# Performance work log

Hardware: AMD Instinct MI355X
Metric: run time of the kernel (lower is better)

Reference implementation:

```python
import jax, jax.numpy as jnp
import numpy as np

N_ITEM, N_USER = 100000, 50000
D, H = 128, 8
DH = D // H
E1, E2 = 500000, 250000
NCNT = 51  # num_cnt_embeddings = cnt.max()+1
EPS = 1e-5


def setup_inputs() -> dict:
    key = jax.random.key(0)
    ks = jax.random.split(key, 32)
    r = lambda i, s: jax.random.normal(ks[i], s, dtype=jnp.float32)
    w = lambda i, s: jax.random.normal(ks[i], s, dtype=jnp.float32) * (1.0 / np.sqrt(s[-1]))
    return {
        # node features
        "ft_item": r(0, (N_ITEM, D)),
        "ft_user": r(1, (N_USER, D)),
        # hetero-level batch norm params (training-mode batch stats)
        "bn_g_item": jnp.ones((D,), jnp.float32), "bn_b_item": jnp.zeros((D,), jnp.float32),
        "bn_g_user": jnp.ones((D,), jnp.float32), "bn_b_user": jnp.zeros((D,), jnp.float32),
        # etype 'i2i' (item -> item), has cnt edge embedding
        "Wq1": w(2, (D, D)), "bq1": jnp.zeros((D,), jnp.float32),
        "Wk1": w(3, (D, D)), "Wv1": w(4, (D, D)),
        "ae1": r(5, (1, D)),
        "emb_cnt1": r(6, (NCNT, D)) * 0.1,
        # etype 'u2i' (user -> item), no cnt
        "Wq2": w(7, (D, D)), "bq2": jnp.zeros((D,), jnp.float32),
        "Wk2": w(8, (D, D)), "Wv2": w(9, (D, D)),
        "ae2": r(10, (1, D)),
        # vtype 'item' output transforms
        "W_agg": w(11, (D, D)), "b_agg": jnp.zeros((D,), jnp.float32),
        "W_self": w(12, (D, D)),
        # edges (eid order)
        "uid1": jax.random.randint(ks[13], (E1,), 0, N_ITEM, dtype=jnp.int32),
        "vid1": jax.random.randint(ks[14], (E1,), 0, N_ITEM, dtype=jnp.int32),
        "cnt1": jax.random.randint(ks[15], (E1,), 0, NCNT, dtype=jnp.int32),
        "uid2": jax.random.randint(ks[16], (E2,), 0, N_USER, dtype=jnp.int32),
        "vid2": jax.random.randint(ks[17], (E2,), 0, N_ITEM, dtype=jnp.int32),
    }


def _bn(x, g, b):
    mu = x.mean(0)
    var = x.var(0)
    return (x - mu) * jax.lax.rsqrt(var + EPS) * g + b


def _edge_scores(q_src, k_dst, uid, vid, attn_e, ft_e=None):
    # u_add_v gather, optional edge feature, gated per-head score [E, H]
    e = q_src[uid] + k_dst[vid]
    if ft_e is not None:
        e = e + ft_e
    e = attn_e * jax.nn.sigmoid(e)
    return e.reshape(-1, H, DH).sum(-1)


def reference(ft_item, ft_user, bn_g_item, bn_b_item, bn_g_user, bn_b_user,
              Wq1, bq1, Wk1, Wv1, ae1, emb_cnt1,
              Wq2, bq2, Wk2, Wv2, ae2,
              W_agg, b_agg, W_self,
              uid1, vid1, cnt1, uid2, vid2):
    xi = _bn(ft_item, bn_g_item, bn_b_item)   # item features (src and dst)
    xu = _bn(ft_user, bn_g_user, bn_b_user)   # user features (src only)

    # etype 'i2i': utype=item, vtype=item (ft_dst = xi, full graph)
    q1 = xi @ Wq1.T + bq1
    k1 = xi @ Wk1.T
    v1 = (xi @ Wv1.T).reshape(N_ITEM, H, DH)
    e1 = _edge_scores(q1, k1, uid1, vid1, ae1, ft_e=emb_cnt1[cnt1])  # [E1, H]

    # etype 'u2i': utype=user, vtype=item
    q2 = xu @ Wq2.T + bq2
    k2 = xi @ Wk2.T
    v2 = (xu @ Wv2.T).reshape(N_USER, H, DH)
    e2 = _edge_scores(q2, k2, uid2, vid2, ae2)  # [E2, H]

    # combined heterograph: offset user src ids by num item src nodes
    src = jnp.concatenate([uid1, uid2 + N_ITEM])
    dst = jnp.concatenate([vid1, vid2])
    val = jnp.concatenate([v1, v2], axis=0)        # [N_ITEM+N_USER, H, DH]
    sc = jnp.concatenate([e1, e2], axis=0)         # [E, H]

    # edge_softmax over incoming edges of each dst node (per head)
    m = jax.lax.stop_gradient(jax.ops.segment_max(sc, dst, num_segments=N_ITEM))
    ex = jnp.exp(sc - m[dst])
    s = jax.ops.segment_sum(ex, dst, num_segments=N_ITEM)
    a = ex / s[dst]                                # [E, H]

    # u_mul_e_sum: weighted scatter-sum of source values to dst
    agg = jax.ops.segment_sum(val[src] * a[:, :, None], dst,
                              num_segments=N_ITEM).reshape(N_ITEM, D)

    return jax.nn.relu(agg @ W_agg.T + b_agg + xi @ W_self.T)
```

## Files before the change

kernel.cpp:

```cpp
#include <hip/hip_runtime.h>
#include <hip/hip_bf16.h>

#define N_ITEM 100000
#define N_USER 50000
#define N_ALL  150000
#define E1N 500000
#define E2N 250000
#define EALL (E1N + E2N)
#define NPAD 100352

static constexpr size_t OFF_STATS = 0;
static constexpr size_t OFF_HIST  = 2048;
static constexpr size_t OFF_SCALE = OFF_HIST + (size_t)NPAD * 4;
static constexpr size_t OFF_M     = OFF_SCALE + 2048;
static constexpr size_t OFF_EMBB  = OFF_M + 64;
static constexpr size_t OFF_WPACK = OFF_EMBB + 13312;
static constexpr size_t OFF_QC    = OFF_WPACK + 8ull * 32768ull;
static constexpr size_t OFF_VC    = OFF_QC + (size_t)N_ALL * 256;
static constexpr size_t OFF_K1    = OFF_VC + (size_t)N_ALL * 256;
static constexpr size_t OFF_K2    = OFF_K1 + (size_t)N_ITEM * 256;
static constexpr size_t OFF_SELF  = OFF_K2 + (size_t)N_ITEM * 256;
static constexpr size_t OFF_START = OFF_SELF + (size_t)N_ITEM * 256;
static constexpr size_t OFF_CURSOR= OFF_START + (size_t)NPAD * 4;
static constexpr size_t OFF_BSUM  = OFF_CURSOR + (size_t)NPAD * 4;
static constexpr size_t OFF_ORD   = OFF_BSUM + 1024;
static constexpr size_t OFF_AGG   = OFF_ORD + (size_t)EALL * 8 + 128;

__device__ __forceinline__ float bf2f(unsigned short u) {
    return __uint_as_float(((unsigned)u) << 16);
}
__device__ __forceinline__ unsigned short f2bf(float f) {
    unsigned u = __float_as_uint(f);
    u += 0x7fffu + ((u >> 16) & 1u);
    return (unsigned short)(u >> 16);
}

typedef __attribute__((ext_vector_type(8))) short bf16x8;
typedef __attribute__((ext_vector_type(4))) float f32x4;

struct ProArgs {
    const float* w[8];
    const float* ft_item;
    const float* ft_user;
    const float* emb;
    const int* vid1;
    const int* vid2;
};
#define PRO_PACK 64
#define PRO_EMB  7
#define PRO_STAT 512
#define PRO_HIST 2930

__global__ __launch_bounds__(256) void prologue(ProArgs A, char* __restrict__ ws) {
    __shared__ float ls[256], ls2[256];
    int b = blockIdx.x, tid = threadIdx.x;
    if (b < PRO_PACK) {
        unsigned short* dst = (unsigned short*)(ws + OFF_WPACK);
        int gid = b * 256 + tid;
        int m = gid >> 11, rem = gid & 2047;
        int t = rem >> 8, kt = (rem >> 6) & 3, lane = rem & 63;
        int n = t * 16 + (lane & 15);
        int k0 = kt * 32 + (lane >> 4) * 8;
        const float* wrow = A.w[m] + n * 128 + k0;
        float4 w0 = *(const float4*)wrow;
        float4 w1 = *(const float4*)(wrow + 4);
        ushort4 o0 = make_ushort4(f2bf(w0.x), f2bf(w0.y), f2bf(w0.z), f2bf(w0.w));
        ushort4 o1 = make_ushort4(f2bf(w1.x), f2bf(w1.y), f2bf(w1.z), f2bf(w1.w));
        *(ushort4*)(dst + (size_t)gid * 8)     = o0;
        *(ushort4*)(dst + (size_t)gid * 8 + 4) = o1;
    } else if (b < PRO_PACK + PRO_EMB) {
        int gid = (b - PRO_PACK) * 256 + tid;
        if (gid * 4 < 51 * 128) {
            float4 v = *(const float4*)(A.emb + gid * 4);
            ushort4 o = make_ushort4(f2bf(v.x), f2bf(v.y), f2bf(v.z), f2bf(v.w));
            *(ushort4*)((unsigned short*)(ws + OFF_EMBB) + gid * 4) = o;
        }
    } else if (b < PRO_PACK + PRO_EMB + PRO_STAT) {
        int bb = b - PRO_PACK - PRO_EMB;
        int type = bb >> 8, xb = bb & 255;
        const float* x = type ? A.ft_user : A.ft_item;
        int N = type ? N_USER : N_ITEM;
        float* sum = (float*)(ws + OFF_STATS) + type * 256;
        float* sq  = sum + 128;
        int c = tid & 127;
        int half = tid >> 7;
        float s = 0.f, s2 = 0.f;
        for (int r = xb * 2 + half; r < N; r += 512) {
            float v = x[(size_t)r * 128 + c];
            s += v; s2 += v * v;
        }
        ls[tid] = s; ls2[tid] = s2;
        __syncthreads();
        if (half == 0) {
            atomicAdd(&sum[c], ls[c] + ls[c + 128]);
            atomicAdd(&sq[c],  ls2[c] + ls2[c + 128]);
        }
    } else {
        int e = (b - PRO_PACK - PRO_EMB - PRO_STAT) * 256 + tid;
        if (e < EALL) {
            int dst = (e < E1N) ? A.vid1[e] : A.vid2[e - E1N];
            atomicAdd((int*)(ws + OFF_HIST) + dst, 1);
        }
    }
}

__global__ __launch_bounds__(1024) void scan_partial(char* __restrict__ ws) {
    __shared__ int sd[1024];
    const int* hist = (const int*)(ws + OFF_HIST);
    int* start  = (int*)(ws + OFF_START);
    int* cursor = (int*)(ws + OFF_CURSOR);
    int* bsum   = (int*)(ws + OFF_BSUM);
    int t = threadIdx.x;
    int gid = blockIdx.x * 1024 + t;
    int v = hist[gid];
    sd[t] = v;
    __syncthreads();
    #pragma unroll
    for (int off = 1; off < 1024; off <<= 1) {
        int x = (t >= off) ? sd[t - off] : 0;
        __syncthreads();
        sd[t] += x;
        __syncthreads();
    }
    int ex = sd[t] - v;
    start[gid] = ex;
    cursor[gid] = ex;
    if (t == 1023) bsum[blockIdx.x] = sd[t];
}

__global__ __launch_bounds__(256) void mid(const float* __restrict__ g_i, const float* __restrict__ b_i,
                                           const float* __restrict__ g_u, const float* __restrict__ b_u,
                                           const float* __restrict__ ae1, const float* __restrict__ ae2,
                                           char* __restrict__ ws) {
    __shared__ int sd[128];
    int t = threadIdx.x;
    if (blockIdx.x == 0) {
        const float* stats = (const float*)(ws + OFF_STATS);
        float* scale = (float*)(ws + OFF_SCALE);
        float* M     = (float*)(ws + OFF_M);
        int type = t >> 7, c = t & 127;
        float N = type ? (float)N_USER : (float)N_ITEM;
        float su = stats[type * 256 + c];
        float sq = stats[type * 256 + 128 + c];
        float mu = su / N;
        float var = sq / N - mu * mu;
        float rstd = rsqrtf(var + 1e-5f);
        float g = type ? g_u[c] : g_i[c];
        float b = type ? b_u[c] : b_i[c];
        scale[type * 256 + c]       = g * rstd;
        scale[type * 256 + 128 + c] = b - mu * g * rstd;
        if (t < 8) {
            float m1 = 0.f, m2 = 0.f;
            for (int j = 0; j < 16; j++) {
                m1 += fmaxf(ae1[t * 16 + j], 0.f);
                m2 += fmaxf(ae2[t * 16 + j], 0.f);
            }
            M[t] = fmaxf(m1, m2);
        }
    } else {
        int* bsum = (int*)(ws + OFF_BSUM);
        int v = 0;
        if (t < 128) { v = (t < 98) ? bsum[t] : 0; sd[t] = v; }
        __syncthreads();
        #pragma unroll
        for (int off = 1; off < 128; off <<= 1) {
            int x = 0;
            if (t < 128 && t >= off) x = sd[t - off];
            __syncthreads();
            if (t < 128) sd[t] += x;
            __syncthreads();
        }
        if (t < 98) bsum[t] = sd[t] - v;
    }
}

__global__ __launch_bounds__(256) void edge_scatter(const int* __restrict__ uid1, const int* __restrict__ vid1,
                                                    const int* __restrict__ cnt1,
                                                    const int* __restrict__ uid2, const int* __restrict__ vid2,
                                                    char* __restrict__ ws) {
    int e = blockIdx.x * 256 + threadIdx.x;
    if (e >= EALL) return;
    int* cursor = (int*)(ws + OFF_CURSOR);
    const int* bsum = (const int*)(ws + OFF_BSUM);
    int2* ord = (int2*)(ws + OFF_ORD);
    int2 rec; int dst;
    if (e < E1N) {
        rec.x = uid1[e]; rec.y = cnt1[e]; dst = vid1[e];
    } else {
        int ee = e - E1N;
        rec.x = N_ITEM + uid2[ee]; rec.y = -1; dst = vid2[ee];
    }
    int pos = atomicAdd(&cursor[dst], 1) + bsum[dst >> 10];
    ord[pos] = rec;
}

struct TArgs {
    const float* x;
    const float* bias0;
    int N;
    int scaleOff;
    int nmat;
    int wtIdx[5];
    unsigned short* out[5];
};

#define TB_I 782
#define TB_U 391
#define SPITCH 136

__global__ __launch_bounds__(256, 5) void transform(TArgs AI, TArgs AU, char* __restrict__ ws) {
    __shared__ unsigned short stg[4][2][16 * SPITCH];
    int b = blockIdx.x;
    const TArgs& A = (b < TB_I) ? AI : AU;
    int blk = (b < TB_I) ? b : b - TB_I;

    const unsigned short* wpack = (const unsigned short*)(ws + OFF_WPACK);
    const float* scaleb = (const float*)(ws + OFF_SCALE) + A.scaleOff;
    int tid = threadIdx.x, lane = tid & 63, wv = tid >> 6;
    int l16 = lane & 15, quad = lane >> 4;
    int base = blk * 128 + wv * 32;

    bf16x8 bfr[2][4];
    #pragma unroll
    for (int kt = 0; kt < 4; kt++) {
        int c0 = kt * 32 + quad * 8;
        float4 sc0 = *(const float4*)(scaleb + c0);
        float4 sc1 = *(const float4*)(scaleb + c0 + 4);
        float4 bi0 = *(const float4*)(scaleb + 128 + c0);
        float4 bi1 = *(const float4*)(scaleb + 128 + c0 + 4);
        #pragma unroll
        for (int it = 0; it < 2; it++) {
            int gr = base + it * 16 + l16;
            bf16x8 f = {0, 0, 0, 0, 0, 0, 0, 0};
            if (gr < A.N) {
                const float* p = A.x + (size_t)gr * 128 + c0;
                float4 v0 = *(const float4*)p;
                float4 v1 = *(const float4*)(p + 4);
                f[0] = (short)f2bf(fmaf(v0.x, sc0.x, bi0.x));
                f[1] = (short)f2bf(fmaf(v0.y, sc0.y, bi0.y));
                f[2] = (short)f2bf(fmaf(v0.z, sc0.z, bi0.z));
                f[3] = (short)f2bf(fmaf(v0.w, sc0.w, bi0.w));
                f[4] = (short)f2bf(fmaf(v1.x, sc1.x, bi1.x));
                f[5] = (short)f2bf(fmaf(v1.y, sc1.y, bi1.y));
                f[6] = (short)f2bf(fmaf(v1.z, sc1.z, bi1.z));
                f[7] = (short)f2bf(fmaf(v1.w, sc1.w, bi1.w));
            }
            bfr[it][kt] = f;
        }
    }

    for (int m = 0; m < A.nmat; m++) {
        const unsigned short* wp = wpack + (size_t)A.wtIdx[m] * 16384;
        unsigned short* outp = A.out[m];
        const float* bias = (m == 0) ? A.bias0 : nullptr;
        #pragma unroll
        for (int it = 0; it < 2; it++) {
            unsigned short* st = stg[wv][it];
            #pragma unroll
            for (int nt = 0; nt < 8; nt++) {
                bf16x8 a4[4];
                #pragma unroll
                for (int kt = 0; kt < 4; kt++)
                    a4[kt] = *(const bf16x8*)(wp + (size_t)((nt * 4 + kt) * 64 + lane) * 8);
                f32x4 acc = {0.f, 0.f, 0.f, 0.f};
                if (bias) {
                    float4 bv = *(const float4*)(bias + nt * 16 + quad * 4);
                    acc[0] = bv.x; acc[1] = bv.y; acc[2] = bv.z; acc[3] = bv.w;
                }
                #pragma unroll
                for (int kt = 0; kt < 4; kt++)
                    acc = __builtin_amdgcn_mfma_f32_16x16x32_bf16(a4[kt], bfr[it][kt], acc, 0, 0, 0);
                ushort4 o = make_ushort4(f2bf(acc[0]), f2bf(acc[1]), f2bf(acc[2]), f2bf(acc[3]));
                *(ushort4*)(st + l16 * SPITCH + nt * 16 + quad * 4) = o;
            }
            #pragma unroll
            for (int i = 0; i < 4; i++) {
                int chunk = i * 64 + lane;
                int row = chunk >> 4, c8 = (chunk & 15) * 8;
                int gr = base + it * 16 + row;
                if (gr < A.N)
                    *(bf16x8*)(outp + (size_t)gr * 128 + c8) = *(const bf16x8*)(st + row * SPITCH + c8);
            }
        }
    }
}

__global__ __launch_bounds__(256, 8) void edge_agg(const float* __restrict__ ae1, const float* __restrict__ ae2,
                                                   char* __restrict__ ws) {
    const unsigned short* qc = (const unsigned short*)(ws + OFF_QC);
    const unsigned short* vc = (const unsigned short*)(ws + OFF_VC);
    const unsigned short* k1 = (const unsigned short*)(ws + OFF_K1);
    const unsigned short* k2 = (const unsigned short*)(ws + OFF_K2);
    const unsigned short* embb = (const unsigned short*)(ws + OFF_EMBB);
    const int* start = (const int*)(ws + OFF_START);
    const int* bsum  = (const int*)(ws + OFF_BSUM);
    const int2* ord = (const int2*)(ws + OFF_ORD);
    const float* M = (const float*)(ws + OFF_M);
    float* agg = (float*)(ws + OFF_AGG);

    int tid = threadIdx.x;
    int lane = tid & 63;
    int half = lane >> 5;
    int l = lane & 31;
    int d0 = l << 2;
    int h = l >> 2;
    int dst = blockIdx.x * 4 + (tid >> 6);
    if (dst >= N_ITEM) return;

    float mh = M[h];
    float4 ae1v = *(const float4*)(ae1 + d0);
    float4 ae2v = *(const float4*)(ae2 + d0);
    ushort4 k1p = *(const ushort4*)(k1 + (size_t)dst * 128 + d0);
    ushort4 k2p = *(const ushort4*)(k2 + (size_t)dst * 128 + d0);
    float4 k1v = make_float4(bf2f(k1p.x), bf2f(k1p.y), bf2f(k1p.z), bf2f(k1p.w));
    float4 k2v = make_float4(bf2f(k2p.x), bf2f(k2p.y), bf2f(k2p.z), bf2f(k2p.w));

    int beg = start[dst] + bsum[dst >> 10];
    int end = start[dst + 1] + bsum[(dst + 1) >> 10];
    float a0 = 0.f, a1 = 0.f, a2 = 0.f, a3 = 0.f, s = 0.f;

    int i = beg + half;
    if (i < end) {
        int2 rec = ord[i];
        while (true) {
            int inext = i + 2;
            int ipf = (inext < end) ? inext : (end - 1);
            int2 recn = ord[ipf];
            bool t1 = rec.y >= 0;
            ushort4 qp = *(const ushort4*)(qc + (size_t)rec.x * 128 + d0);
            ushort4 vp = *(const ushort4*)(vc + (size_t)rec.x * 128 + d0);
            ushort4 ep = *(const ushort4*)(embb + (size_t)(t1 ? rec.y : 0) * 128 + d0);
            float x0 = bf2f(qp.x) + (t1 ? k1v.x + bf2f(ep.x) : k2v.x);
            float x1 = bf2f(qp.y) + (t1 ? k1v.y + bf2f(ep.y) : k2v.y);
            float x2 = bf2f(qp.z) + (t1 ? k1v.z + bf2f(ep.z) : k2v.z);
            float x3 = bf2f(qp.w) + (t1 ? k1v.w + bf2f(ep.w) : k2v.w);
            float4 ae = t1 ? ae1v : ae2v;
            float t = ae.x * __builtin_amdgcn_rcpf(1.f + __expf(-x0))
                    + ae.y * __builtin_amdgcn_rcpf(1.f + __expf(-x1))
                    + ae.z * __builtin_amdgcn_rcpf(1.f + __expf(-x2))
                    + ae.w * __builtin_amdgcn_rcpf(1.f + __expf(-x3));
            t += __shfl_xor(t, 1);
            t += __shfl_xor(t, 2);
            float ex = __expf(t - mh);
            s += ex;
            a0 = fmaf(ex, bf2f(vp.x), a0);
            a1 = fmaf(ex, bf2f(vp.y), a1);
            a2 = fmaf(ex, bf2f(vp.z), a2);
            a3 = fmaf(ex, bf2f(vp.w), a3);
            if (inext >= end) break;
            i = inext; rec = recn;
        }
    }
    s  += __shfl_xor(s, 32);
    a0 += __shfl_xor(a0, 32);
    a1 += __shfl_xor(a1, 32);
    a2 += __shfl_xor(a2, 32);
    a3 += __shfl_xor(a3, 32);
    if (half == 0) {
        float inv = (s > 0.f) ? __builtin_amdgcn_rcpf(s) : 0.f;
        float4 o = make_float4(a0 * inv, a1 * inv, a2 * inv, a3 * inv);
        *(float4*)(agg + (size_t)dst * 128 + d0) = o;
    }
}

#define FPITCH 132

__global__ __launch_bounds__(256) void final_mfma(const float* __restrict__ b_agg,
                                                  float* __restrict__ out, char* __restrict__ ws) {
    __shared__ float stg[4][16 * FPITCH];
    const float* agg = (const float*)(ws + OFF_AGG);
    const unsigned short* selft = (const unsigned short*)(ws + OFF_SELF);
    const unsigned short* wp = (const unsigned short*)(ws + OFF_WPACK) + 7ull * 16384;
    int tid = threadIdx.x, lane = tid & 63, wv = tid >> 6;
    int l16 = lane & 15, quad = lane >> 4;
    int base = blockIdx.x * 256 + wv * 64;
    float* st = stg[wv];

    bf16x8 bfr[4][4];
    #pragma unroll
    for (int it = 0; it < 4; it++) {
        int gr = base + it * 16 + l16;
        #pragma unroll
        for (int kt = 0; kt < 4; kt++) {
            bf16x8 f = {0, 0, 0, 0, 0, 0, 0, 0};
            if (gr < N_ITEM) {
                const float* p = agg + (size_t)gr * 128 + kt * 32 + quad * 8;
                float4 v0 = *(const float4*)p;
                float4 v1 = *(const float4*)(p + 4);
                f[0] = (short)f2bf(v0.x); f[1] = (short)f2bf(v0.y);
                f[2] = (short)f2bf(v0.z); f[3] = (short)f2bf(v0.w);
                f[4] = (short)f2bf(v1.x); f[5] = (short)f2bf(v1.y);
                f[6] = (short)f2bf(v1.z); f[7] = (short)f2bf(v1.w);
            }
            bfr[it][kt] = f;
        }
    }

    #pragma unroll
    for (int it = 0; it < 4; it++) {
        #pragma unroll
        for (int nt = 0; nt < 8; nt++) {
            bf16x8 a4[4];
            #pragma unroll
            for (int kt = 0; kt < 4; kt++)
                a4[kt] = *(const bf16x8*)(wp + (size_t)((nt * 4 + kt) * 64 + lane) * 8);
            float4 bv = *(const float4*)(b_agg + nt * 16 + quad * 4);
            f32x4 acc = {bv.x, bv.y, bv.z, bv.w};
            #pragma unroll
            for (int kt = 0; kt < 4; kt++)
                acc = __builtin_amdgcn_mfma_f32_16x16x32_bf16(a4[kt], bfr[it][kt], acc, 0, 0, 0);
            *(f32x4*)(st + l16 * FPITCH + nt * 16 + quad * 4) = acc;
        }
        #pragma unroll
        for (int i = 0; i < 8; i++) {
            int chunk = i * 64 + lane;
            int row = chunk >> 5, c4 = (chunk & 31) * 4;
            int gr = base + it * 16 + row;
            if (gr < N_ITEM) {
                float4 v = *(const float4*)(st + row * FPITCH + c4);
                size_t idx = (size_t)gr * 128 + c4;
                ushort4 sf = *(const ushort4*)(selft + idx);
                float4 o;
                o.x = fmaxf(v.x + bf2f(sf.x), 0.f);
                o.y = fmaxf(v.y + bf2f(sf.y), 0.f);
                o.z = fmaxf(v.z + bf2f(sf.z), 0.f);
                o.w = fmaxf(v.w + bf2f(sf.w), 0.f);
                *(float4*)(out + idx) = o;
            }
        }
    }
}

extern "C" void kernel_launch(void* const* d_in, const int* in_sizes, int n_in,
                              void* d_out, int out_size, void* d_ws, size_t ws_size,
                              hipStream_t stream) {
    char* ws = (char*)d_ws;

    const float* ft_item = (const float*)d_in[0];
    const float* ft_user = (const float*)d_in[1];
    const float* bng_i = (const float*)d_in[2];
    const float* bnb_i = (const float*)d_in[3];
    const float* bng_u = (const float*)d_in[4];
    const float* bnb_u = (const float*)d_in[5];
    const float* Wq1 = (const float*)d_in[6];
    const float* bq1 = (const float*)d_in[7];
    const float* Wk1 = (const float*)d_in[8];
    const float* Wv1 = (const float*)d_in[9];
    const float* ae1 = (const float*)d_in[10];
    const float* emb = (const float*)d_in[11];
    const float* Wq2 = (const float*)d_in[12];
    const float* bq2 = (const float*)d_in[13];
    const float* Wk2 = (const float*)d_in[14];
    const float* Wv2 = (const float*)d_in[15];
    const float* ae2 = (const float*)d_in[16];
    const float* W_agg = (const float*)d_in[17];
    const float* b_agg = (const float*)d_in[18];
    const float* W_self = (const float*)d_in[19];
    const int* uid1 = (const int*)d_in[20];
    const int* vid1 = (const int*)d_in[21];
    const int* cnt1 = (const int*)d_in[22];
    const int* uid2 = (const int*)d_in[23];
    const int* vid2 = (const int*)d_in[24];
    float* out = (float*)d_out;

    hipMemsetAsync(ws + OFF_STATS, 0, 2048 + (size_t)NPAD * 4, stream);

    ProArgs pa;
    pa.w[0] = Wq1; pa.w[1] = Wk1; pa.w[2] = Wv1; pa.w[3] = Wk2;
    pa.w[4] = W_self; pa.w[5] = Wq2; pa.w[6] = Wv2; pa.w[7] = W_agg;
    pa.ft_item = ft_item; pa.ft_user = ft_user; pa.emb = emb;
    pa.vid1 = vid1; pa.vid2 = vid2;
    prologue<<<PRO_PACK + PRO_EMB + PRO_STAT + PRO_HIST, 256, 0, stream>>>(pa, ws);

    scan_partial<<<98, 1024, 0, stream>>>(ws);

    mid<<<2, 256, 0, stream>>>(bng_i, bnb_i, bng_u, bnb_u, ae1, ae2, ws);

    edge_scatter<<<(EALL + 255) / 256, 256, 0, stream>>>(uid1, vid1, cnt1, uid2, vid2, ws);

    TArgs ti, tu;
    ti.x = ft_item; ti.bias0 = bq1; ti.N = N_ITEM; ti.scaleOff = 0; ti.nmat = 5;
    ti.wtIdx[0] = 0; ti.wtIdx[1] = 1; ti.wtIdx[2] = 2; ti.wtIdx[3] = 3; ti.wtIdx[4] = 4;
    unsigned short* QC = (unsigned short*)(ws + OFF_QC);
    unsigned short* VC = (unsigned short*)(ws + OFF_VC);
    ti.out[0] = QC;
    ti.out[1] = (unsigned short*)(ws + OFF_K1);
    ti.out[2] = VC;
    ti.out[3] = (unsigned short*)(ws + OFF_K2);
    ti.out[4] = (unsigned short*)(ws + OFF_SELF);
    tu.x = ft_user; tu.bias0 = bq2; tu.N = N_USER; tu.scaleOff = 256; tu.nmat = 2;
    tu.wtIdx[0] = 5; tu.wtIdx[1] = 6; tu.wtIdx[2] = 0; tu.wtIdx[3] = 0; tu.wtIdx[4] = 0;
    tu.out[0] = QC + (size_t)N_ITEM * 128;
    tu.out[1] = VC + (size_t)N_ITEM * 128;
    tu.out[2] = tu.out[3] = tu.out[4] = tu.out[0];
    transform<<<TB_I + TB_U, 256, 0, stream>>>(ti, tu, ws);

    edge_agg<<<(N_ITEM + 3) / 4, 256, 0, stream>>>(ae1, ae2, ws);

    final_mfma<<<(N_ITEM + 255) / 256, 256, 0, stream>>>(b_agg, out, ws);
}
```

Before: 505.9 us.

## Fuse edge scatter into transform launch and vectorize prologue stats and histogram

Removes the separate edge_scatter kernel and runs it as extra blocks appended to the transform grid, so the CSR bucketing overlaps with the GEMM work and one launch disappears. The prologue is reordered so the heavier stats and histogram blocks are dispatched first. Batch-norm statistics now use float4 loads with warp-shuffle reduction over fewer blocks, and the histogram processes four edges per thread with int4 loads. The trade-off is extra branching and register pressure in the transform kernel, plus a different atomic ordering in the scatter.

```diff
diff --git a/kernel.cpp b/kernel.cpp
--- a/kernel.cpp
+++ b/kernel.cpp
@@ -46,17 +46,65 @@
     const int* vid1;
     const int* vid2;
 };
+#define PRO_STAT 384
+#define PRO_HIST 733
 #define PRO_PACK 64
 #define PRO_EMB  7
-#define PRO_STAT 512
-#define PRO_HIST 2930
 
 __global__ __launch_bounds__(256) void prologue(ProArgs A, char* __restrict__ ws) {
-    __shared__ float ls[256], ls2[256];
+    __shared__ float r1[4][128], r2[4][128];
     int b = blockIdx.x, tid = threadIdx.x;
-    if (b < PRO_PACK) {
+    if (b < PRO_STAT) {
+        int type = (b >= 256) ? 1 : 0;
+        int xb = type ? (b - 256) : b;
+        int nb = type ? 128 : 256;
+        const float* x = type ? A.ft_user : A.ft_item;
+        int N = type ? N_USER : N_ITEM;
+        float* sum = (float*)(ws + OFF_STATS) + type * 256;
+        float* sq  = sum + 128;
+        int c4 = (tid & 31) * 4;
+        int rg = tid >> 5;
+        int step = nb * 8;
+        float s0 = 0.f, s1 = 0.f, s2 = 0.f, s3 = 0.f;
+        float q0 = 0.f, q1 = 0.f, q2 = 0.f, q3 = 0.f;
+        #pragma unroll 4
+        for (int r = xb * 8 + rg; r < N; r += step) {
+            float4 v = *(const float4*)(x + (size_t)r * 128 + c4);
+            s0 += v.x; s1 += v.y; s2 += v.z; s3 += v.w;
+            q0 = fmaf(v.x, v.x, q0); q1 = fmaf(v.y, v.y, q1);
+            q2 = fmaf(v.z, v.z, q2); q3 = fmaf(v.w, v.w, q3);
+        }
+        s0 += __shfl_xor(s0, 32); s1 += __shfl_xor(s1, 32);
+        s2 += __shfl_xor(s2, 32); s3 += __shfl_xor(s3, 32);
+        q0 += __shfl_xor(q0, 32); q1 += __shfl_xor(q1, 32);
+        q2 += __shfl_xor(q2, 32); q3 += __shfl_xor(q3, 32);
+        int wv = tid >> 6;
+        if ((tid & 63) < 32) {
+            *(float4*)&r1[wv][c4] = make_float4(s0, s1, s2, s3);
+            *(float4*)&r2[wv][c4] = make_float4(q0, q1, q2, q3);
+        }
+        __syncthreads();
+        if (tid < 128) {
+            float a  = r1[0][tid] + r1[1][tid] + r1[2][tid] + r1[3][tid];
+            float bb = r2[0][tid] + r2[1][tid] + r2[2][tid] + r2[3][tid];
+            atomicAdd(&sum[tid], a);
+            atomicAdd(&sq[tid], bb);
+        }
+    } else if (b < PRO_STAT + PRO_HIST) {
+        int e4 = ((b - PRO_STAT) * 256 + tid) * 4;
+        if (e4 < EALL) {
+            int* hist = (int*)(ws + OFF_HIST);
+            int4 v;
+            if (e4 < E1N) v = *(const int4*)(A.vid1 + e4);
+            else          v = *(const int4*)(A.vid2 + (e4 - E1N));
+            atomicAdd(&hist[v.x], 1);
+            atomicAdd(&hist[v.y], 1);
+            atomicAdd(&hist[v.z], 1);
+            atomicAdd(&hist[v.w], 1);
+        }
+    } else if (b < PRO_STAT + PRO_HIST + PRO_PACK) {
         unsigned short* dst = (unsigned short*)(ws + OFF_WPACK);
-        int gid = b * 256 + tid;
+        int gid = (b - PRO_STAT - PRO_HIST) * 256 + tid;
         int m = gid >> 11, rem = gid & 2047;
         int t = rem >> 8, kt = (rem >> 6) & 3, lane = rem & 63;
         int n = t * 16 + (lane & 15);
@@ -68,38 +116,12 @@
         ushort4 o1 = make_ushort4(f2bf(w1.x), f2bf(w1.y), f2bf(w1.z), f2bf(w1.w));
         *(ushort4*)(dst + (size_t)gid * 8)     = o0;
         *(ushort4*)(dst + (size_t)gid * 8 + 4) = o1;
-    } else if (b < PRO_PACK + PRO_EMB) {
-        int gid = (b - PRO_PACK) * 256 + tid;
+    } else {
+        int gid = (b - PRO_STAT - PRO_HIST - PRO_PACK) * 256 + tid;
         if (gid * 4 < 51 * 128) {
             float4 v = *(const float4*)(A.emb + gid * 4);
             ushort4 o = make_ushort4(f2bf(v.x), f2bf(v.y), f2bf(v.z), f2bf(v.w));
             *(ushort4*)((unsigned short*)(ws + OFF_EMBB) + gid * 4) = o;
-        }
-    } else if (b < PRO_PACK + PRO_EMB + PRO_STAT) {
-        int bb = b - PRO_PACK - PRO_EMB;
-        int type = bb >> 8, xb = bb & 255;
-        const float* x = type ? A.ft_user : A.ft_item;
-        int N = type ? N_USER : N_ITEM;
-        float* sum = (float*)(ws + OFF_STATS) + type * 256;
-        float* sq  = sum + 128;
-        int c = tid & 127;
-        int half = tid >> 7;
-        float s = 0.f, s2 = 0.f;
-        for (int r = xb * 2 + half; r < N; r += 512) {
-            float v = x[(size_t)r * 128 + c];
-            s += v; s2 += v * v;
-        }
-        ls[tid] = s; ls2[tid] = s2;
-        __syncthreads();
-        if (half == 0) {
-            atomicAdd(&sum[c], ls[c] + ls[c + 128]);
-            atomicAdd(&sq[c],  ls2[c] + ls2[c + 128]);
-        }
-    } else {
-        int e = (b - PRO_PACK - PRO_EMB - PRO_STAT) * 256 + tid;
-        if (e < EALL) {
-            int dst = (e < E1N) ? A.vid1[e] : A.vid2[e - E1N];
-            atomicAdd((int*)(ws + OFF_HIST) + dst, 1);
         }
     }
 }
@@ -174,26 +196,6 @@
     }
 }
 
-__global__ __launch_bounds__(256) void edge_scatter(const int* __restrict__ uid1, const int* __restrict__ vid1,
-                                                    const int* __restrict__ cnt1,
-                                                    const int* __restrict__ uid2, const int* __restrict__ vid2,
-                                                    char* __restrict__ ws) {
-    int e = blockIdx.x * 256 + threadIdx.x;
-    if (e >= EALL) return;
-    int* cursor = (int*)(ws + OFF_CURSOR);
-    const int* bsum = (const int*)(ws + OFF_BSUM);
-    int2* ord = (int2*)(ws + OFF_ORD);
-    int2 rec; int dst;
-    if (e < E1N) {
-        rec.x = uid1[e]; rec.y = cnt1[e]; dst = vid1[e];
-    } else {
-        int ee = e - E1N;
-        rec.x = N_ITEM + uid2[ee]; rec.y = -1; dst = vid2[ee];
-    }
-    int pos = atomicAdd(&cursor[dst], 1) + bsum[dst >> 10];
-    ord[pos] = rec;
-}
-
 struct TArgs {
     const float* x;
     const float* bias0;
@@ -203,14 +205,50 @@
     int wtIdx[5];
     unsigned short* out[5];
 };
+struct ScArgs {
+    const int* uid1; const int* vid1; const int* cnt1;
+    const int* uid2; const int* vid2;
+};
 
 #define TB_I 782
 #define TB_U 391
+#define SC_B 733
 #define SPITCH 136
 
-__global__ __launch_bounds__(256, 5) void transform(TArgs AI, TArgs AU, char* __restrict__ ws) {
+__global__ __launch_bounds__(256, 5) void transform(TArgs AI, TArgs AU, ScArgs S, char* __restrict__ ws) {
     __shared__ unsigned short stg[4][2][16 * SPITCH];
     int b = blockIdx.x;
+    if (b >= TB_I + TB_U) {
+        int e0 = ((b - TB_I - TB_U) * 256 + threadIdx.x) * 4;
+        if (e0 < EALL) {
+            int* cursor = (int*)(ws + OFF_CURSOR);
+            const int* bsum = (const int*)(ws + OFF_BSUM);
+            int2* ord = (int2*)(ws + OFF_ORD);
+            int4 u, c, d;
+            if (e0 < E1N) {
+                u = *(const int4*)(S.uid1 + e0);
+                d = *(const int4*)(S.vid1 + e0);
+                c = *(const int4*)(S.cnt1 + e0);
+            } else {
+                int ee = e0 - E1N;
+                u = *(const int4*)(S.uid2 + ee);
+                d = *(const int4*)(S.vid2 + ee);
+                u.x += N_ITEM; u.y += N_ITEM; u.z += N_ITEM; u.w += N_ITEM;
+                c = make_int4(-1, -1, -1, -1);
+            }
+            int us[4] = {u.x, u.y, u.z, u.w};
+            int ds[4] = {d.x, d.y, d.z, d.w};
+            int cs[4] = {c.x, c.y, c.z, c.w};
+            #pragma unroll
+            for (int j = 0; j < 4; j++) {
+                int dst = ds[j];
+                int pos = atomicAdd(&cursor[dst], 1) + bsum[dst >> 10];
+                int2 rec; rec.x = us[j]; rec.y = cs[j];
+                ord[pos] = rec;
+            }
+        }
+        return;
+    }
     const TArgs& A = (b < TB_I) ? AI : AU;
     int blk = (b < TB_I) ? b : b - TB_I;
 
@@ -470,13 +508,11 @@
     pa.w[4] = W_self; pa.w[5] = Wq2; pa.w[6] = Wv2; pa.w[7] = W_agg;
     pa.ft_item = ft_item; pa.ft_user = ft_user; pa.emb = emb;
     pa.vid1 = vid1; pa.vid2 = vid2;
-    prologue<<<PRO_PACK + PRO_EMB + PRO_STAT + PRO_HIST, 256, 0, stream>>>(pa, ws);
+    prologue<<<PRO_STAT + PRO_HIST + PRO_PACK + PRO_EMB, 256, 0, stream>>>(pa, ws);
 
     scan_partial<<<98, 1024, 0, stream>>>(ws);
 
     mid<<<2, 256, 0, stream>>>(bng_i, bnb_i, bng_u, bnb_u, ae1, ae2, ws);
-
-    edge_scatter<<<(EALL + 255) / 256, 256, 0, stream>>>(uid1, vid1, cnt1, uid2, vid2, ws);
 
     TArgs ti, tu;
     ti.x = ft_item; ti.bias0 = bq1; ti.N = N_ITEM; ti.scaleOff = 0; ti.nmat = 5;
@@ -493,7 +529,9 @@
     tu.out[0] = QC + (size_t)N_ITEM * 128;
     tu.out[1] = VC + (size_t)N_ITEM * 128;
     tu.out[2] = tu.out[3] = tu.out[4] = tu.out[0];
-    transform<<<TB_I + TB_U, 256, 0, stream>>>(ti, tu, ws);
+    ScArgs sa;
+    sa.uid1 = uid1; sa.vid1 = vid1; sa.cnt1 = cnt1; sa.uid2 = uid2; sa.vid2 = vid2;
+    transform<<<TB_I + TB_U + SC_B, 256, 0, stream>>>(ti, tu, sa, ws);
 
     edge_agg<<<(N_ITEM + 3) / 4, 256, 0, stream>>>(ae1, ae2, ws);
 
```

After: 435.8 us. 13.9% less time.
